# Kernel tuning notes

Hardware: AMD Instinct MI355X
Metric: run time of the kernel (lower is better)

The kernel has to match this reference:

```python
import jax, jax.numpy as jnp
import numpy as np

N = 70000
H = 8
E = 1120000
B = 8


def setup_inputs() -> dict:
    key = jax.random.key(0)
    ks = jax.random.split(key, 12)
    inp = {
        'calcium_t': jax.random.normal(ks[0], (B, N), jnp.float32),
        'hidden': jax.random.normal(ks[1], (B, N, H), jnp.float32),
        'src': jax.random.randint(ks[2], (E,), 0, N, jnp.int32),
        'tgt': jax.random.randint(ks[3], (E,), 0, N, jnp.int32),
        'W_z_values': jax.random.normal(ks[4], (E, H), jnp.float32) * 0.01,
        'W_r_values': jax.random.normal(ks[5], (E, H), jnp.float32) * 0.01,
        'W_h_values': jax.random.normal(ks[6], (E, H), jnp.float32) * 0.01,
        'U_z': jax.random.normal(ks[7], (N, H, H), jnp.float32) * 0.01,
        'U_r': jax.random.normal(ks[8], (N, H, H), jnp.float32) * 0.01,
        'U_h': jax.random.normal(ks[9], (N, H, H), jnp.float32) * 0.01,
        'b_z': jnp.zeros((N, H), jnp.float32),
        'b_r': jnp.zeros((N, H), jnp.float32),
        'b_h': jnp.zeros((N, H), jnp.float32),
        'output_projection': jax.random.normal(ks[10], (H,), jnp.float32),
    }
    return inp


def _sparse_matmul(values, src, tgt, calcium):
    # out[b, n, h] = sum over edges e with tgt[e]==n of values[e,h]*calcium[b,src[e]]
    # (identical to coalesced COO mm: duplicate (row,col) values are summed)
    gathered = calcium.T[src]                      # (E, B)
    contrib = gathered[:, :, None] * values[:, None, :]  # (E, B, H)
    out = jax.ops.segment_sum(contrib, tgt, num_segments=N)  # (N, B, H)
    return jnp.transpose(out, (1, 0, 2))           # (B, N, H)


def reference(calcium_t, hidden, src, tgt, W_z_values, W_r_values, W_h_values,
              U_z, U_r, U_h, b_z, b_r, b_h, output_projection):
    inp_z = _sparse_matmul(W_z_values, src, tgt, calcium_t)
    inp_r = _sparse_matmul(W_r_values, src, tgt, calcium_t)
    inp_h = _sparse_matmul(W_h_values, src, tgt, calcium_t)

    rec_z = jnp.einsum('bnh,nhi->bni', hidden, U_z)
    rec_r = jnp.einsum('bnh,nhi->bni', hidden, U_r)
    z = jax.nn.sigmoid(inp_z + rec_z + b_z[None])
    r = jax.nn.sigmoid(inp_r + rec_r + b_r[None])

    rec_h = jnp.einsum('bnh,nhi->bni', r * hidden, U_h)
    h_tilde = jnp.tanh(inp_h + rec_h + b_h[None])

    hidden_new = (1.0 - z) * hidden + z * h_tilde
    calcium_t1 = jax.nn.relu(jnp.einsum('bnh,h->bn', hidden_new, output_projection))
    return calcium_t1, hidden_new
```

## Files before the change

kernel.cpp:

```cpp
#include <hip/hip_runtime.h>


typedef float f2 __attribute__((ext_vector_type(2)));

__device__ __forceinline__ float fast_sigmoid(float x) {
    return 1.0f / (1.0f + __expf(-x));
}
__device__ __forceinline__ float fast_tanh(float x) {
    return 2.0f / (1.0f + __expf(-2.0f * x)) - 1.0f;
}

__device__ __forceinline__ unsigned bfr(float x) {
    unsigned u = __float_as_uint(x);
    return (u + 0x7fffu + ((u >> 16) & 1u)) >> 16;
}
__device__ __forceinline__ uint4 pack8(float4 a, float4 b) {
    uint4 r;
    r.x = bfr(a.x) | (bfr(a.y) << 16);
    r.y = bfr(a.z) | (bfr(a.w) << 16);
    r.z = bfr(b.x) | (bfr(b.y) << 16);
    r.w = bfr(b.z) | (bfr(b.w) << 16);
    return r;
}

#define BFMA2(acc, p, c2)                                                      \
    {                                                                          \
        f2 w;                                                                  \
        w.x = __uint_as_float((p).x << 16);                                    \
        w.y = __uint_as_float((p).x & 0xffff0000u);                            \
        acc[0] = __builtin_elementwise_fma(w, c2, acc[0]);                     \
        w.x = __uint_as_float((p).y << 16);                                    \
        w.y = __uint_as_float((p).y & 0xffff0000u);                            \
        acc[1] = __builtin_elementwise_fma(w, c2, acc[1]);                     \
        w.x = __uint_as_float((p).z << 16);                                    \
        w.y = __uint_as_float((p).z & 0xffff0000u);                            \
        acc[2] = __builtin_elementwise_fma(w, c2, acc[2]);                     \
        w.x = __uint_as_float((p).w << 16);                                    \
        w.y = __uint_as_float((p).w & 0xffff0000u);                            \
        acc[3] = __builtin_elementwise_fma(w, c2, acc[3]);                     \
    }

__global__ void hist_kernel(const int* __restrict__ tgt, int* __restrict__ cnt,
                            int* __restrict__ rank, const float* __restrict__ cal,
                            float* __restrict__ calT, int N, int E) {
    int i = blockIdx.x * blockDim.x + threadIdx.x;
    if (i <= N) {
        float4* o = (float4*)(calT + (size_t)i * 8);
        if (i == N) {
            o[0] = make_float4(0.f, 0.f, 0.f, 0.f);
            o[1] = make_float4(0.f, 0.f, 0.f, 0.f);
        } else {
            float v[8];
#pragma unroll
            for (int b = 0; b < 8; ++b) v[b] = cal[(size_t)b * N + i];
            o[0] = make_float4(v[0], v[1], v[2], v[3]);
            o[1] = make_float4(v[4], v[5], v[6], v[7]);
        }
    }
    int base = i * 4;
    if (base + 3 < E) {
        int4 t = *(const int4*)(tgt + base);
        int4 r;
        r.x = atomicAdd(&cnt[t.x], 1);
        r.y = atomicAdd(&cnt[t.y], 1);
        r.z = atomicAdd(&cnt[t.z], 1);
        r.w = atomicAdd(&cnt[t.w], 1);
        *(int4*)(rank + base) = r;
    } else {
        for (int k = base; k < E; ++k) rank[k] = atomicAdd(&cnt[tgt[k]], 1);
    }
}

__global__ __launch_bounds__(256) void alloc_kernel(const int* __restrict__ cnt,
                                                    int2* __restrict__ rowCnt,
                                                    int* __restrict__ cursor, int N) {
    __shared__ int waveSum[4];
    const int n = blockIdx.x * 256 + threadIdx.x;
    const int lane = threadIdx.x & 63;
    const int wid = threadIdx.x >> 6;
    int c = (n < N) ? cnt[n] : 0;
    int pre = c;
#pragma unroll
    for (int off = 1; off < 64; off <<= 1) {
        int v = __shfl_up(pre, off, 64);
        if (lane >= off) pre += v;
    }
    if (lane == 63) waveSum[wid] = pre;
    __syncthreads();
    if (threadIdx.x == 0) {
        int s0 = waveSum[0], s1 = waveSum[1], s2 = waveSum[2], s3 = waveSum[3];
        int base = atomicAdd(cursor, s0 + s1 + s2 + s3);
        waveSum[0] = base;
        waveSum[1] = base + s0;
        waveSum[2] = base + s0 + s1;
        waveSum[3] = base + s0 + s1 + s2;
    }
    __syncthreads();
    if (n < N) rowCnt[n] = make_int2(waveSum[wid] + (pre - c), c);
}

__global__ __launch_bounds__(256) void pack_store(
    const int* __restrict__ src, const int* __restrict__ tgt,
    const int* __restrict__ rank, const int2* __restrict__ rowCnt,
    const float* __restrict__ Wz, const float* __restrict__ Wr,
    const float* __restrict__ Wh, const float* __restrict__ calT,
    uint4* __restrict__ recs, int E) {
    int gid = blockIdx.x * 256 + threadIdx.x;
    int e = gid >> 2;
    int q = gid & 3;
    if (e >= E) return;
    int t = tgt[e];
    int pos = rowCnt[t].x + rank[e];
    const float* base;
    size_t off;
    if (q == 0)      { base = Wz;   off = (size_t)e * 8; }
    else if (q == 1) { base = Wr;   off = (size_t)e * 8; }
    else if (q == 2) { base = Wh;   off = (size_t)e * 8; }
    else             { base = calT; off = (size_t)src[e] * 8; }
    const float4* p = (const float4*)(base + off);
    float4 a = p[0], b = p[1];
    recs[(size_t)pos * 4 + q] = pack8(a, b);
}

__device__ __forceinline__ float rscatter(float v[8], int lane) {
    const bool s0 = (lane & 8) != 0;
    const bool s1 = (lane & 16) != 0;
    const bool s2 = (lane & 32) != 0;
    float w0, w1, w2, w3, x0, x1;
    { float k = s0 ? v[1] : v[0], g = s0 ? v[0] : v[1]; w0 = k + __shfl_xor(g, 8, 64); }
    { float k = s0 ? v[3] : v[2], g = s0 ? v[2] : v[3]; w1 = k + __shfl_xor(g, 8, 64); }
    { float k = s0 ? v[5] : v[4], g = s0 ? v[4] : v[5]; w2 = k + __shfl_xor(g, 8, 64); }
    { float k = s0 ? v[7] : v[6], g = s0 ? v[6] : v[7]; w3 = k + __shfl_xor(g, 8, 64); }
    { float k = s1 ? w1 : w0, g = s1 ? w0 : w1; x0 = k + __shfl_xor(g, 16, 64); }
    { float k = s1 ? w3 : w2, g = s1 ? w2 : w3; x1 = k + __shfl_xor(g, 16, 64); }
    float k = s2 ? x1 : x0, g = s2 ? x0 : x1;
    return k + __shfl_xor(g, 32, 64);
}

__global__ __launch_bounds__(256) void gru_main(
    const float* __restrict__ hidden, const uint4* __restrict__ recs,
    const float* __restrict__ Uz, const float* __restrict__ Ur,
    const float* __restrict__ Uh, const float* __restrict__ bz,
    const float* __restrict__ br, const float* __restrict__ bh,
    const float* __restrict__ proj, const int2* __restrict__ rowCnt,
    float* __restrict__ outCal, float* __restrict__ outHid, int N) {
    const int lane = threadIdx.x & 63;
    const int n = blockIdx.x * 4 + (threadIdx.x >> 6);
    if (n >= N) return;
    const int s = lane >> 3;
    const int b = lane & 7;

    const int2 rc = rowCnt[n];
    const int start = rc.x;
    const int end = rc.x + rc.y;

    const float hvS = hidden[((b * N + n) << 3) + s];
    const int ub = (n << 6) + (s << 3);
    const f2* uz2 = (const f2*)(Uz + ub);
    const f2* ur2 = (const f2*)(Ur + ub);
    const f2* uh2 = (const f2*)(Uh + ub);
    f2 uzr[4], urr[4], uhr[4];
#pragma unroll
    for (int k = 0; k < 4; ++k) {
        uzr[k] = uz2[k];
        urr[k] = ur2[k];
        uhr[k] = uh2[k];
    }
    const float bzS = bz[(n << 3) + s];
    const float brS = br[(n << 3) + s];
    const float bhS = bh[(n << 3) + s];
    const float pjS = proj[s];

    f2 az2[4], ar2[4], ah2[4];
#pragma unroll
    for (int k = 0; k < 4; ++k) {
        az2[k] = (f2){0.0f, 0.0f};
        ar2[k] = (f2){0.0f, 0.0f};
        ah2[k] = (f2){0.0f, 0.0f};
    }

    const unsigned short* recsH = (const unsigned short*)recs;
    for (int j = start + s; j < end; j += 8) {
        const uint4* rp = recs + (size_t)j * 4;
        uint4 pz = rp[0];
        uint4 pr = rp[1];
        uint4 ph = rp[2];
        unsigned cb = recsH[((size_t)j << 5) + 24 + b];
        float c = __uint_as_float(cb << 16);
        f2 c2 = {c, c};
        BFMA2(az2, pz, c2);
        BFMA2(ar2, pr, c2);
        BFMA2(ah2, ph, c2);
    }

    f2 hv2 = {hvS, hvS};
#pragma unroll
    for (int k = 0; k < 4; ++k) {
        az2[k] = __builtin_elementwise_fma(uzr[k], hv2, az2[k]);
        ar2[k] = __builtin_elementwise_fma(urr[k], hv2, ar2[k]);
    }

    float az[8], ar[8];
#pragma unroll
    for (int k = 0; k < 4; ++k) {
        az[2 * k] = az2[k].x; az[2 * k + 1] = az2[k].y;
        ar[2 * k] = ar2[k].x; ar[2 * k + 1] = ar2[k].y;
    }
    float AZ = rscatter(az, lane);
    float AR = rscatter(ar, lane);
    float z = fast_sigmoid(AZ + bzS);
    float r = fast_sigmoid(AR + brS);
    float rhS = r * hvS;

    f2 rh2 = {rhS, rhS};
#pragma unroll
    for (int k = 0; k < 4; ++k) {
        ah2[k] = __builtin_elementwise_fma(uhr[k], rh2, ah2[k]);
    }
    float ah[8];
#pragma unroll
    for (int k = 0; k < 4; ++k) {
        ah[2 * k] = ah2[k].x; ah[2 * k + 1] = ah2[k].y;
    }
    float AH = rscatter(ah, lane);
    float ht = fast_tanh(AH + bhS);
    float hn = (1.0f - z) * hvS + z * ht;

    float cv = hn * pjS;
    cv += __shfl_xor(cv, 8, 64);
    cv += __shfl_xor(cv, 16, 64);
    cv += __shfl_xor(cv, 32, 64);

    outHid[((b * N + n) << 3) + s] = hn;
    if (s == 0) outCal[b * N + n] = fmaxf(cv, 0.0f);
}

extern "C" void kernel_launch(void* const* d_in, const int* in_sizes, int n_in,
                              void* d_out, int out_size, void* d_ws, size_t ws_size,
                              hipStream_t stream) {
    const float* calcium = (const float*)d_in[0];
    const float* hidden  = (const float*)d_in[1];
    const int*   src     = (const int*)d_in[2];
    const int*   tgt     = (const int*)d_in[3];
    const float* Wz      = (const float*)d_in[4];
    const float* Wr      = (const float*)d_in[5];
    const float* Wh      = (const float*)d_in[6];
    const float* Uz      = (const float*)d_in[7];
    const float* Ur      = (const float*)d_in[8];
    const float* Uh      = (const float*)d_in[9];
    const float* bz      = (const float*)d_in[10];
    const float* br      = (const float*)d_in[11];
    const float* bh      = (const float*)d_in[12];
    const float* proj    = (const float*)d_in[13];

    const int E = in_sizes[2];
    const int H = in_sizes[13];
    const int N = in_sizes[10] / H;
    (void)n_in; (void)out_size; (void)ws_size;

    float* out = (float*)d_out;
    float* outCal = out;
    float* outHid = out + (size_t)in_sizes[0];

    char* ws = (char*)d_ws;
    int*   cnt    = (int*)ws;
    int*   cursor = (int*)(ws + (448 << 10));
    int2*  rowCnt = (int2*)(ws + (512 << 10));
    int*   rank   = (int*)(ws + (1280 << 10));
    float* calT   = (float*)(ws + (5888 << 10));
    uint4* recs   = (uint4*)(ws + (8320 << 10));

    hipMemsetAsync(ws, 0, (448 << 10) + 4, stream);

    int histThreads = (E + 3) / 4;
    hist_kernel<<<(histThreads + 255) / 256, 256, 0, stream>>>(
        tgt, cnt, rank, calcium, calT, N, E);
    alloc_kernel<<<(N + 255) / 256, 256, 0, stream>>>(cnt, rowCnt, cursor, N);
    {
        long long pthreads = (long long)E * 4;
        pack_store<<<(int)((pthreads + 255) / 256), 256, 0, stream>>>(
            src, tgt, rank, rowCnt, Wz, Wr, Wh, calT, recs, E);
    }
    gru_main<<<(N + 3) / 4, 256, 0, stream>>>(
        hidden, recs, Uz, Ur, Uh, bz, br, bh, proj,
        rowCnt, outCal, outHid, N);
}
```

Measured before the change: 180.7 us.

## Map two nodes per wavefront with four edge slots per node in GRU kernel

The main GRU kernel now gives each 64-lane wavefront two nodes, 32 lanes each, instead of one node. Each lane handles two hidden slots (lo/hi), and the edge loop strides by 4 instead of 8. The transpose-reduce now needs only two shuffle stages, and the grid is halved. The goal is less lane waste on nodes with few edges (average degree 16) and fewer shuffles, at the cost of more registers per lane and fewer edge-parallel lanes per node.

```diff
diff --git a/kernel.cpp b/kernel.cpp
--- a/kernel.cpp
+++ b/kernel.cpp
@@ -122,19 +122,16 @@
     recs[(size_t)pos * 4 + q] = pack8(a, b);
 }
 
-__device__ __forceinline__ float rscatter(float v[8], int lane) {
-    const bool s0 = (lane & 8) != 0;
-    const bool s1 = (lane & 16) != 0;
-    const bool s2 = (lane & 32) != 0;
-    float w0, w1, w2, w3, x0, x1;
-    { float k = s0 ? v[1] : v[0], g = s0 ? v[0] : v[1]; w0 = k + __shfl_xor(g, 8, 64); }
-    { float k = s0 ? v[3] : v[2], g = s0 ? v[2] : v[3]; w1 = k + __shfl_xor(g, 8, 64); }
-    { float k = s0 ? v[5] : v[4], g = s0 ? v[4] : v[5]; w2 = k + __shfl_xor(g, 8, 64); }
-    { float k = s0 ? v[7] : v[6], g = s0 ? v[6] : v[7]; w3 = k + __shfl_xor(g, 8, 64); }
-    { float k = s1 ? w1 : w0, g = s1 ? w0 : w1; x0 = k + __shfl_xor(g, 16, 64); }
-    { float k = s1 ? w3 : w2, g = s1 ? w2 : w3; x1 = k + __shfl_xor(g, 16, 64); }
-    float k = s2 ? x1 : x0, g = s2 ? x0 : x1;
-    return k + __shfl_xor(g, 32, 64);
+__device__ __forceinline__ f2 rscatter2(const f2 v[4], bool s0, bool s1) {
+    float w0, w1, w2, w3;
+    { float k = s0 ? v[0].y : v[0].x, g = s0 ? v[0].x : v[0].y; w0 = k + __shfl_xor(g, 8, 64); }
+    { float k = s0 ? v[1].y : v[1].x, g = s0 ? v[1].x : v[1].y; w1 = k + __shfl_xor(g, 8, 64); }
+    { float k = s0 ? v[2].y : v[2].x, g = s0 ? v[2].x : v[2].y; w2 = k + __shfl_xor(g, 8, 64); }
+    { float k = s0 ? v[3].y : v[3].x, g = s0 ? v[3].x : v[3].y; w3 = k + __shfl_xor(g, 8, 64); }
+    f2 r;
+    { float k = s1 ? w1 : w0, g = s1 ? w0 : w1; r.x = k + __shfl_xor(g, 16, 64); }
+    { float k = s1 ? w3 : w2, g = s1 ? w2 : w3; r.y = k + __shfl_xor(g, 16, 64); }
+    return r;
 }
 
 __global__ __launch_bounds__(256) void gru_main(
@@ -145,31 +142,35 @@
     const float* __restrict__ proj, const int2* __restrict__ rowCnt,
     float* __restrict__ outCal, float* __restrict__ outHid, int N) {
     const int lane = threadIdx.x & 63;
-    const int n = blockIdx.x * 4 + (threadIdx.x >> 6);
+    const int wid = threadIdx.x >> 6;
+    const int nn = lane >> 5;
+    const int s = (lane >> 3) & 3;
+    const int b = lane & 7;
+    const int n = blockIdx.x * 8 + wid * 2 + nn;
     if (n >= N) return;
-    const int s = lane >> 3;
-    const int b = lane & 7;
+
+    const bool s0 = (lane & 8) != 0;
+    const bool s1 = (lane & 16) != 0;
 
     const int2 rc = rowCnt[n];
     const int start = rc.x;
     const int end = rc.x + rc.y;
 
-    const float hvS = hidden[((b * N + n) << 3) + s];
-    const int ub = (n << 6) + (s << 3);
-    const f2* uz2 = (const f2*)(Uz + ub);
-    const f2* ur2 = (const f2*)(Ur + ub);
-    const f2* uh2 = (const f2*)(Uh + ub);
-    f2 uzr[4], urr[4], uhr[4];
-#pragma unroll
-    for (int k = 0; k < 4; ++k) {
-        uzr[k] = uz2[k];
-        urr[k] = ur2[k];
-        uhr[k] = uh2[k];
-    }
-    const float bzS = bz[(n << 3) + s];
-    const float brS = br[(n << 3) + s];
-    const float bhS = bh[(n << 3) + s];
-    const float pjS = proj[s];
+    const size_t hb = ((size_t)(b * N + n)) << 3;
+    const float hv_lo = hidden[hb + s];
+    const float hv_hi = hidden[hb + s + 4];
+    const int ub_lo = (n << 6) + (s << 3);
+    const int ub_hi = ub_lo + 32;
+    f2 uzl[4], uzh[4], url[4], urh[4];
+#pragma unroll
+    for (int k = 0; k < 4; ++k) {
+        uzl[k] = ((const f2*)(Uz + ub_lo))[k];
+        uzh[k] = ((const f2*)(Uz + ub_hi))[k];
+        url[k] = ((const f2*)(Ur + ub_lo))[k];
+        urh[k] = ((const f2*)(Ur + ub_hi))[k];
+    }
+    const float bz_lo = bz[(n << 3) + s], bz_hi = bz[(n << 3) + s + 4];
+    const float br_lo = br[(n << 3) + s], br_hi = br[(n << 3) + s + 4];
 
     f2 az2[4], ar2[4], ah2[4];
 #pragma unroll
@@ -180,7 +181,7 @@
     }
 
     const unsigned short* recsH = (const unsigned short*)recs;
-    for (int j = start + s; j < end; j += 8) {
+    for (int j = start + s; j < end; j += 4) {
         const uint4* rp = recs + (size_t)j * 4;
         uint4 pz = rp[0];
         uint4 pr = rp[1];
@@ -193,46 +194,52 @@
         BFMA2(ah2, ph, c2);
     }
 
-    f2 hv2 = {hvS, hvS};
-#pragma unroll
-    for (int k = 0; k < 4; ++k) {
-        az2[k] = __builtin_elementwise_fma(uzr[k], hv2, az2[k]);
-        ar2[k] = __builtin_elementwise_fma(urr[k], hv2, ar2[k]);
-    }
-
-    float az[8], ar[8];
-#pragma unroll
-    for (int k = 0; k < 4; ++k) {
-        az[2 * k] = az2[k].x; az[2 * k + 1] = az2[k].y;
-        ar[2 * k] = ar2[k].x; ar[2 * k + 1] = ar2[k].y;
-    }
-    float AZ = rscatter(az, lane);
-    float AR = rscatter(ar, lane);
-    float z = fast_sigmoid(AZ + bzS);
-    float r = fast_sigmoid(AR + brS);
-    float rhS = r * hvS;
-
-    f2 rh2 = {rhS, rhS};
-#pragma unroll
-    for (int k = 0; k < 4; ++k) {
-        ah2[k] = __builtin_elementwise_fma(uhr[k], rh2, ah2[k]);
-    }
-    float ah[8];
-#pragma unroll
-    for (int k = 0; k < 4; ++k) {
-        ah[2 * k] = ah2[k].x; ah[2 * k + 1] = ah2[k].y;
-    }
-    float AH = rscatter(ah, lane);
-    float ht = fast_tanh(AH + bhS);
-    float hn = (1.0f - z) * hvS + z * ht;
-
-    float cv = hn * pjS;
+    f2 hvl2 = {hv_lo, hv_lo};
+    f2 hvh2 = {hv_hi, hv_hi};
+#pragma unroll
+    for (int k = 0; k < 4; ++k) {
+        az2[k] = __builtin_elementwise_fma(uzl[k], hvl2, az2[k]);
+        az2[k] = __builtin_elementwise_fma(uzh[k], hvh2, az2[k]);
+        ar2[k] = __builtin_elementwise_fma(url[k], hvl2, ar2[k]);
+        ar2[k] = __builtin_elementwise_fma(urh[k], hvh2, ar2[k]);
+    }
+
+    f2 uhl[4], uhh[4];
+#pragma unroll
+    for (int k = 0; k < 4; ++k) {
+        uhl[k] = ((const f2*)(Uh + ub_lo))[k];
+        uhh[k] = ((const f2*)(Uh + ub_hi))[k];
+    }
+    const float bh_lo = bh[(n << 3) + s], bh_hi = bh[(n << 3) + s + 4];
+    const float pj_lo = proj[s], pj_hi = proj[s + 4];
+
+    f2 AZ = rscatter2(az2, s0, s1);
+    f2 AR = rscatter2(ar2, s0, s1);
+    float z_lo = fast_sigmoid(AZ.x + bz_lo);
+    float z_hi = fast_sigmoid(AZ.y + bz_hi);
+    float r_lo = fast_sigmoid(AR.x + br_lo);
+    float r_hi = fast_sigmoid(AR.y + br_hi);
+
+    f2 rhl2 = {r_lo * hv_lo, r_lo * hv_lo};
+    f2 rhh2 = {r_hi * hv_hi, r_hi * hv_hi};
+#pragma unroll
+    for (int k = 0; k < 4; ++k) {
+        ah2[k] = __builtin_elementwise_fma(uhl[k], rhl2, ah2[k]);
+        ah2[k] = __builtin_elementwise_fma(uhh[k], rhh2, ah2[k]);
+    }
+    f2 AH = rscatter2(ah2, s0, s1);
+    float ht_lo = fast_tanh(AH.x + bh_lo);
+    float ht_hi = fast_tanh(AH.y + bh_hi);
+    float hn_lo = (1.0f - z_lo) * hv_lo + z_lo * ht_lo;
+    float hn_hi = (1.0f - z_hi) * hv_hi + z_hi * ht_hi;
+
+    float cv = hn_lo * pj_lo + hn_hi * pj_hi;
     cv += __shfl_xor(cv, 8, 64);
     cv += __shfl_xor(cv, 16, 64);
-    cv += __shfl_xor(cv, 32, 64);
-
-    outHid[((b * N + n) << 3) + s] = hn;
-    if (s == 0) outCal[b * N + n] = fmaxf(cv, 0.0f);
+
+    outHid[hb + s] = hn_lo;
+    outHid[hb + s + 4] = hn_hi;
+    if ((lane & 24) == 0) outCal[b * N + n] = fmaxf(cv, 0.0f);
 }
 
 extern "C" void kernel_launch(void* const* d_in, const int* in_sizes, int n_in,
@@ -281,7 +288,7 @@
         pack_store<<<(int)((pthreads + 255) / 256), 256, 0, stream>>>(
             src, tgt, rank, rowCnt, Wz, Wr, Wh, calT, recs, E);
     }
-    gru_main<<<(N + 3) / 4, 256, 0, stream>>>(
+    gru_main<<<(N + 7) / 8, 256, 0, stream>>>(
         hidden, recs, Uz, Ur, Uh, bz, br, bh, proj,
         rowCnt, outCal, outHid, N);
 }
```

New measurement: 182.9 us. Within noise of the previous version (+1.3%).

## Fuse memset and four kernels into one cooperative persistent kernel

Applied to the files above, without the earlier changes.

Replaces the memset and the histogram, prefix-allocation, record-packing and GRU kernels with a single cooperative kernel. The phases are separated by grid-wide syncs and use grid-stride loops over a grid sized by occupancy. The aim is to remove the per-launch and inter-kernel gap overhead. In exchange it adds the cost of grid barriers and caps the number of resident blocks, which may reduce latency hiding in the memory-bound gather and scatter phases.

```diff
diff --git a/kernel.cpp b/kernel.cpp
--- a/kernel.cpp
+++ b/kernel.cpp
@@ -1,7 +1,37 @@
 #include <hip/hip_runtime.h>
+#include <hip/hip_cooperative_groups.h>
+
+namespace cg = cooperative_groups;
 
 
 typedef float f2 __attribute__((ext_vector_type(2)));
+
+struct GruParams {
+    const int* src;
+    const int* tgt;
+    const float* Wz;
+    const float* Wr;
+    const float* Wh;
+    const float* cal;
+    const float* hidden;
+    const float* Uz;
+    const float* Ur;
+    const float* Uh;
+    const float* bz;
+    const float* br;
+    const float* bh;
+    const float* proj;
+    int* cnt;
+    int* cursor;
+    int2* rowCnt;
+    int* rank;
+    float* calT;
+    uint4* recs;
+    float* outCal;
+    float* outHid;
+    int N;
+    int E;
+};
 
 __device__ __forceinline__ float fast_sigmoid(float x) {
     return 1.0f / (1.0f + __expf(-x));
@@ -40,88 +70,6 @@
         acc[3] = __builtin_elementwise_fma(w, c2, acc[3]);                     \
     }
 
-__global__ void hist_kernel(const int* __restrict__ tgt, int* __restrict__ cnt,
-                            int* __restrict__ rank, const float* __restrict__ cal,
-                            float* __restrict__ calT, int N, int E) {
-    int i = blockIdx.x * blockDim.x + threadIdx.x;
-    if (i <= N) {
-        float4* o = (float4*)(calT + (size_t)i * 8);
-        if (i == N) {
-            o[0] = make_float4(0.f, 0.f, 0.f, 0.f);
-            o[1] = make_float4(0.f, 0.f, 0.f, 0.f);
-        } else {
-            float v[8];
-#pragma unroll
-            for (int b = 0; b < 8; ++b) v[b] = cal[(size_t)b * N + i];
-            o[0] = make_float4(v[0], v[1], v[2], v[3]);
-            o[1] = make_float4(v[4], v[5], v[6], v[7]);
-        }
-    }
-    int base = i * 4;
-    if (base + 3 < E) {
-        int4 t = *(const int4*)(tgt + base);
-        int4 r;
-        r.x = atomicAdd(&cnt[t.x], 1);
-        r.y = atomicAdd(&cnt[t.y], 1);
-        r.z = atomicAdd(&cnt[t.z], 1);
-        r.w = atomicAdd(&cnt[t.w], 1);
-        *(int4*)(rank + base) = r;
-    } else {
-        for (int k = base; k < E; ++k) rank[k] = atomicAdd(&cnt[tgt[k]], 1);
-    }
-}
-
-__global__ __launch_bounds__(256) void alloc_kernel(const int* __restrict__ cnt,
-                                                    int2* __restrict__ rowCnt,
-                                                    int* __restrict__ cursor, int N) {
-    __shared__ int waveSum[4];
-    const int n = blockIdx.x * 256 + threadIdx.x;
-    const int lane = threadIdx.x & 63;
-    const int wid = threadIdx.x >> 6;
-    int c = (n < N) ? cnt[n] : 0;
-    int pre = c;
-#pragma unroll
-    for (int off = 1; off < 64; off <<= 1) {
-        int v = __shfl_up(pre, off, 64);
-        if (lane >= off) pre += v;
-    }
-    if (lane == 63) waveSum[wid] = pre;
-    __syncthreads();
-    if (threadIdx.x == 0) {
-        int s0 = waveSum[0], s1 = waveSum[1], s2 = waveSum[2], s3 = waveSum[3];
-        int base = atomicAdd(cursor, s0 + s1 + s2 + s3);
-        waveSum[0] = base;
-        waveSum[1] = base + s0;
-        waveSum[2] = base + s0 + s1;
-        waveSum[3] = base + s0 + s1 + s2;
-    }
-    __syncthreads();
-    if (n < N) rowCnt[n] = make_int2(waveSum[wid] + (pre - c), c);
-}
-
-__global__ __launch_bounds__(256) void pack_store(
-    const int* __restrict__ src, const int* __restrict__ tgt,
-    const int* __restrict__ rank, const int2* __restrict__ rowCnt,
-    const float* __restrict__ Wz, const float* __restrict__ Wr,
-    const float* __restrict__ Wh, const float* __restrict__ calT,
-    uint4* __restrict__ recs, int E) {
-    int gid = blockIdx.x * 256 + threadIdx.x;
-    int e = gid >> 2;
-    int q = gid & 3;
-    if (e >= E) return;
-    int t = tgt[e];
-    int pos = rowCnt[t].x + rank[e];
-    const float* base;
-    size_t off;
-    if (q == 0)      { base = Wz;   off = (size_t)e * 8; }
-    else if (q == 1) { base = Wr;   off = (size_t)e * 8; }
-    else if (q == 2) { base = Wh;   off = (size_t)e * 8; }
-    else             { base = calT; off = (size_t)src[e] * 8; }
-    const float4* p = (const float4*)(base + off);
-    float4 a = p[0], b = p[1];
-    recs[(size_t)pos * 4 + q] = pack8(a, b);
-}
-
 __device__ __forceinline__ float rscatter(float v[8], int lane) {
     const bool s0 = (lane & 8) != 0;
     const bool s1 = (lane & 16) != 0;
@@ -137,151 +85,240 @@
     return k + __shfl_xor(g, 32, 64);
 }
 
-__global__ __launch_bounds__(256) void gru_main(
-    const float* __restrict__ hidden, const uint4* __restrict__ recs,
-    const float* __restrict__ Uz, const float* __restrict__ Ur,
-    const float* __restrict__ Uh, const float* __restrict__ bz,
-    const float* __restrict__ br, const float* __restrict__ bh,
-    const float* __restrict__ proj, const int2* __restrict__ rowCnt,
-    float* __restrict__ outCal, float* __restrict__ outHid, int N) {
-    const int lane = threadIdx.x & 63;
-    const int n = blockIdx.x * 4 + (threadIdx.x >> 6);
-    if (n >= N) return;
-    const int s = lane >> 3;
-    const int b = lane & 7;
-
-    const int2 rc = rowCnt[n];
-    const int start = rc.x;
-    const int end = rc.x + rc.y;
-
-    const float hvS = hidden[((b * N + n) << 3) + s];
-    const int ub = (n << 6) + (s << 3);
-    const f2* uz2 = (const f2*)(Uz + ub);
-    const f2* ur2 = (const f2*)(Ur + ub);
-    const f2* uh2 = (const f2*)(Uh + ub);
-    f2 uzr[4], urr[4], uhr[4];
-#pragma unroll
-    for (int k = 0; k < 4; ++k) {
-        uzr[k] = uz2[k];
-        urr[k] = ur2[k];
-        uhr[k] = uh2[k];
-    }
-    const float bzS = bz[(n << 3) + s];
-    const float brS = br[(n << 3) + s];
-    const float bhS = bh[(n << 3) + s];
-    const float pjS = proj[s];
-
-    f2 az2[4], ar2[4], ah2[4];
-#pragma unroll
-    for (int k = 0; k < 4; ++k) {
-        az2[k] = (f2){0.0f, 0.0f};
-        ar2[k] = (f2){0.0f, 0.0f};
-        ah2[k] = (f2){0.0f, 0.0f};
-    }
-
-    const unsigned short* recsH = (const unsigned short*)recs;
-    for (int j = start + s; j < end; j += 8) {
-        const uint4* rp = recs + (size_t)j * 4;
-        uint4 pz = rp[0];
-        uint4 pr = rp[1];
-        uint4 ph = rp[2];
-        unsigned cb = recsH[((size_t)j << 5) + 24 + b];
-        float c = __uint_as_float(cb << 16);
-        f2 c2 = {c, c};
-        BFMA2(az2, pz, c2);
-        BFMA2(ar2, pr, c2);
-        BFMA2(ah2, ph, c2);
-    }
-
-    f2 hv2 = {hvS, hvS};
-#pragma unroll
-    for (int k = 0; k < 4; ++k) {
-        az2[k] = __builtin_elementwise_fma(uzr[k], hv2, az2[k]);
-        ar2[k] = __builtin_elementwise_fma(urr[k], hv2, ar2[k]);
-    }
-
-    float az[8], ar[8];
-#pragma unroll
-    for (int k = 0; k < 4; ++k) {
-        az[2 * k] = az2[k].x; az[2 * k + 1] = az2[k].y;
-        ar[2 * k] = ar2[k].x; ar[2 * k + 1] = ar2[k].y;
-    }
-    float AZ = rscatter(az, lane);
-    float AR = rscatter(ar, lane);
-    float z = fast_sigmoid(AZ + bzS);
-    float r = fast_sigmoid(AR + brS);
-    float rhS = r * hvS;
-
-    f2 rh2 = {rhS, rhS};
-#pragma unroll
-    for (int k = 0; k < 4; ++k) {
-        ah2[k] = __builtin_elementwise_fma(uhr[k], rh2, ah2[k]);
-    }
-    float ah[8];
-#pragma unroll
-    for (int k = 0; k < 4; ++k) {
-        ah[2 * k] = ah2[k].x; ah[2 * k + 1] = ah2[k].y;
-    }
-    float AH = rscatter(ah, lane);
-    float ht = fast_tanh(AH + bhS);
-    float hn = (1.0f - z) * hvS + z * ht;
-
-    float cv = hn * pjS;
-    cv += __shfl_xor(cv, 8, 64);
-    cv += __shfl_xor(cv, 16, 64);
-    cv += __shfl_xor(cv, 32, 64);
-
-    outHid[((b * N + n) << 3) + s] = hn;
-    if (s == 0) outCal[b * N + n] = fmaxf(cv, 0.0f);
+__global__ __launch_bounds__(256) void mega(GruParams P) {
+    cg::grid_group grid = cg::this_grid();
+    const int tid = blockIdx.x * 256 + threadIdx.x;
+    const int stride = gridDim.x * 256;
+    const int N = P.N;
+    const int E = P.E;
+
+    for (int i = tid; i < N; i += stride) P.cnt[i] = 0;
+    if (tid == 0) *P.cursor = 0;
+    grid.sync();
+
+    {
+        const int histWork = (E + 3) / 4;
+        for (int i = tid; i < histWork; i += stride) {
+            if (i <= N) {
+                float4* o = (float4*)(P.calT + (size_t)i * 8);
+                if (i == N) {
+                    o[0] = make_float4(0.f, 0.f, 0.f, 0.f);
+                    o[1] = make_float4(0.f, 0.f, 0.f, 0.f);
+                } else {
+                    float v[8];
+#pragma unroll
+                    for (int b = 0; b < 8; ++b) v[b] = P.cal[(size_t)b * N + i];
+                    o[0] = make_float4(v[0], v[1], v[2], v[3]);
+                    o[1] = make_float4(v[4], v[5], v[6], v[7]);
+                }
+            }
+            int base = i * 4;
+            if (base + 3 < E) {
+                int4 t = *(const int4*)(P.tgt + base);
+                int4 r;
+                r.x = atomicAdd(&P.cnt[t.x], 1);
+                r.y = atomicAdd(&P.cnt[t.y], 1);
+                r.z = atomicAdd(&P.cnt[t.z], 1);
+                r.w = atomicAdd(&P.cnt[t.w], 1);
+                *(int4*)(P.rank + base) = r;
+            } else {
+                for (int k = base; k < E; ++k) rank_tail:;
+                for (int k = base; k < E; ++k) P.rank[k] = atomicAdd(&P.cnt[P.tgt[k]], 1);
+            }
+        }
+    }
+    grid.sync();
+
+    {
+        __shared__ int waveSum[4];
+        const int lane = threadIdx.x & 63;
+        const int wid = threadIdx.x >> 6;
+        const int nChunks = (N + 255) >> 8;
+        for (int ch = blockIdx.x; ch < nChunks; ch += gridDim.x) {
+            const int n = ch * 256 + threadIdx.x;
+            int c = (n < N) ? P.cnt[n] : 0;
+            int pre = c;
+#pragma unroll
+            for (int off = 1; off < 64; off <<= 1) {
+                int v = __shfl_up(pre, off, 64);
+                if (lane >= off) pre += v;
+            }
+            if (lane == 63) waveSum[wid] = pre;
+            __syncthreads();
+            if (threadIdx.x == 0) {
+                int s0 = waveSum[0], s1 = waveSum[1], s2 = waveSum[2], s3 = waveSum[3];
+                int base = atomicAdd(P.cursor, s0 + s1 + s2 + s3);
+                waveSum[0] = base;
+                waveSum[1] = base + s0;
+                waveSum[2] = base + s0 + s1;
+                waveSum[3] = base + s0 + s1 + s2;
+            }
+            __syncthreads();
+            if (n < N) P.rowCnt[n] = make_int2(waveSum[wid] + (pre - c), c);
+            __syncthreads();
+        }
+    }
+    grid.sync();
+
+    {
+        const int total = E * 4;
+        for (int g = tid; g < total; g += stride) {
+            int e = g >> 2;
+            int q = g & 3;
+            int t = P.tgt[e];
+            int pos = P.rowCnt[t].x + P.rank[e];
+            const float* base;
+            size_t off;
+            if (q == 0)      { base = P.Wz;   off = (size_t)e * 8; }
+            else if (q == 1) { base = P.Wr;   off = (size_t)e * 8; }
+            else if (q == 2) { base = P.Wh;   off = (size_t)e * 8; }
+            else             { base = P.calT; off = (size_t)P.src[e] * 8; }
+            const float4* p = (const float4*)(base + off);
+            float4 a = p[0], b = p[1];
+            P.recs[(size_t)pos * 4 + q] = pack8(a, b);
+        }
+    }
+    grid.sync();
+
+    {
+        const int lane = threadIdx.x & 63;
+        const int s = lane >> 3;
+        const int b = lane & 7;
+        const unsigned short* recsH = (const unsigned short*)P.recs;
+        for (int n0 = blockIdx.x * 4; n0 < N; n0 += gridDim.x * 4) {
+            const int n = n0 + (threadIdx.x >> 6);
+            if (n >= N) continue;
+
+            const int2 rc = P.rowCnt[n];
+            const int start = rc.x;
+            const int end = rc.x + rc.y;
+
+            const size_t hb = ((size_t)(b * N + n)) << 3;
+            const float hvS = P.hidden[hb + s];
+            const int ub = (n << 6) + (s << 3);
+            f2 uzr[4], urr[4], uhr[4];
+#pragma unroll
+            for (int k = 0; k < 4; ++k) {
+                uzr[k] = ((const f2*)(P.Uz + ub))[k];
+                urr[k] = ((const f2*)(P.Ur + ub))[k];
+                uhr[k] = ((const f2*)(P.Uh + ub))[k];
+            }
+            const float bzS = P.bz[(n << 3) + s];
+            const float brS = P.br[(n << 3) + s];
+            const float bhS = P.bh[(n << 3) + s];
+            const float pjS = P.proj[s];
+
+            f2 az2[4], ar2[4], ah2[4];
+#pragma unroll
+            for (int k = 0; k < 4; ++k) {
+                az2[k] = (f2){0.0f, 0.0f};
+                ar2[k] = (f2){0.0f, 0.0f};
+                ah2[k] = (f2){0.0f, 0.0f};
+            }
+
+            for (int j = start + s; j < end; j += 8) {
+                const uint4* rp = P.recs + (size_t)j * 4;
+                uint4 pz = rp[0];
+                uint4 pr = rp[1];
+                uint4 ph = rp[2];
+                unsigned cb = recsH[((size_t)j << 5) + 24 + b];
+                float c = __uint_as_float(cb << 16);
+                f2 c2 = {c, c};
+                BFMA2(az2, pz, c2);
+                BFMA2(ar2, pr, c2);
+                BFMA2(ah2, ph, c2);
+            }
+
+            f2 hv2 = {hvS, hvS};
+#pragma unroll
+            for (int k = 0; k < 4; ++k) {
+                az2[k] = __builtin_elementwise_fma(uzr[k], hv2, az2[k]);
+                ar2[k] = __builtin_elementwise_fma(urr[k], hv2, ar2[k]);
+            }
+
+            float az[8], ar[8];
+#pragma unroll
+            for (int k = 0; k < 4; ++k) {
+                az[2 * k] = az2[k].x; az[2 * k + 1] = az2[k].y;
+                ar[2 * k] = ar2[k].x; ar[2 * k + 1] = ar2[k].y;
+            }
+            float AZ = rscatter(az, lane);
+            float AR = rscatter(ar, lane);
+            float z = fast_sigmoid(AZ + bzS);
+            float r = fast_sigmoid(AR + brS);
+            float rhS = r * hvS;
+
+            f2 rh2 = {rhS, rhS};
+#pragma unroll
+            for (int k = 0; k < 4; ++k) {
+                ah2[k] = __builtin_elementwise_fma(uhr[k], rh2, ah2[k]);
+            }
+            float ah[8];
+#pragma unroll
+            for (int k = 0; k < 4; ++k) {
+                ah[2 * k] = ah2[k].x; ah[2 * k + 1] = ah2[k].y;
+            }
+            float AH = rscatter(ah, lane);
+            float ht = fast_tanh(AH + bhS);
+            float hn = (1.0f - z) * hvS + z * ht;
+
+            float cv = hn * pjS;
+            cv += __shfl_xor(cv, 8, 64);
+            cv += __shfl_xor(cv, 16, 64);
+            cv += __shfl_xor(cv, 32, 64);
+
+            P.outHid[hb + s] = hn;
+            if (s == 0) P.outCal[b * N + n] = fmaxf(cv, 0.0f);
+        }
+    }
 }
 
 extern "C" void kernel_launch(void* const* d_in, const int* in_sizes, int n_in,
                               void* d_out, int out_size, void* d_ws, size_t ws_size,
                               hipStream_t stream) {
-    const float* calcium = (const float*)d_in[0];
-    const float* hidden  = (const float*)d_in[1];
-    const int*   src     = (const int*)d_in[2];
-    const int*   tgt     = (const int*)d_in[3];
-    const float* Wz      = (const float*)d_in[4];
-    const float* Wr      = (const float*)d_in[5];
-    const float* Wh      = (const float*)d_in[6];
-    const float* Uz      = (const float*)d_in[7];
-    const float* Ur      = (const float*)d_in[8];
-    const float* Uh      = (const float*)d_in[9];
-    const float* bz      = (const float*)d_in[10];
-    const float* br      = (const float*)d_in[11];
-    const float* bh      = (const float*)d_in[12];
-    const float* proj    = (const float*)d_in[13];
-
-    const int E = in_sizes[2];
+    GruParams P;
+    P.cal    = (const float*)d_in[0];
+    P.hidden = (const float*)d_in[1];
+    P.src    = (const int*)d_in[2];
+    P.tgt    = (const int*)d_in[3];
+    P.Wz     = (const float*)d_in[4];
+    P.Wr     = (const float*)d_in[5];
+    P.Wh     = (const float*)d_in[6];
+    P.Uz     = (const float*)d_in[7];
+    P.Ur     = (const float*)d_in[8];
+    P.Uh     = (const float*)d_in[9];
+    P.bz     = (const float*)d_in[10];
+    P.br     = (const float*)d_in[11];
+    P.bh     = (const float*)d_in[12];
+    P.proj   = (const float*)d_in[13];
+
+    P.E = in_sizes[2];
     const int H = in_sizes[13];
-    const int N = in_sizes[10] / H;
+    P.N = in_sizes[10] / H;
     (void)n_in; (void)out_size; (void)ws_size;
 
     float* out = (float*)d_out;
-    float* outCal = out;
-    float* outHid = out + (size_t)in_sizes[0];
+    P.outCal = out;
+    P.outHid = out + (size_t)in_sizes[0];
 
     char* ws = (char*)d_ws;
-    int*   cnt    = (int*)ws;
-    int*   cursor = (int*)(ws + (448 << 10));
-    int2*  rowCnt = (int2*)(ws + (512 << 10));
-    int*   rank   = (int*)(ws + (1280 << 10));
-    float* calT   = (float*)(ws + (5888 << 10));
-    uint4* recs   = (uint4*)(ws + (8320 << 10));
-
-    hipMemsetAsync(ws, 0, (448 << 10) + 4, stream);
-
-    int histThreads = (E + 3) / 4;
-    hist_kernel<<<(histThreads + 255) / 256, 256, 0, stream>>>(
-        tgt, cnt, rank, calcium, calT, N, E);
-    alloc_kernel<<<(N + 255) / 256, 256, 0, stream>>>(cnt, rowCnt, cursor, N);
-    {
-        long long pthreads = (long long)E * 4;
-        pack_store<<<(int)((pthreads + 255) / 256), 256, 0, stream>>>(
-            src, tgt, rank, rowCnt, Wz, Wr, Wh, calT, recs, E);
-    }
-    gru_main<<<(N + 3) / 4, 256, 0, stream>>>(
-        hidden, recs, Uz, Ur, Uh, bz, br, bh, proj,
-        rowCnt, outCal, outHid, N);
-}
+    P.cnt    = (int*)ws;
+    P.cursor = (int*)(ws + (448 << 10));
+    P.rowCnt = (int2*)(ws + (512 << 10));
+    P.rank   = (int*)(ws + (1280 << 10));
+    P.calT   = (float*)(ws + (5888 << 10));
+    P.recs   = (uint4*)(ws + (8320 << 10));
+
+    int occ = 0;
+    hipOccupancyMaxActiveBlocksPerMultiprocessor(&occ, (const void*)mega, 256, 0);
+    if (occ < 1) occ = 1;
+    int numCU = 256;
+    hipDeviceGetAttribute(&numCU, hipDeviceAttributeMultiprocessorCount, 0);
+    int gridBlocks = occ * numCU;
+    int maxUseful = (P.N + 3) / 4;
+    if (gridBlocks > maxUseful) gridBlocks = maxUseful;
+
+    void* args[] = { &P };
+    hipLaunchCooperativeKernel((const void*)mega, dim3(gridBlocks), dim3(256),
+                               args, 0, stream);
+}
```

After: 455.2 us. 152% more time.
